# Kernel tuning notes

Hardware: AMD Instinct MI355X
Metric: run time of the kernel (lower is better)

The kernel has to match this reference:

```python
import jax, jax.numpy as jnp
import numpy as np

N = 100000    # nodes
E = 1600000   # edges (avg degree 16)
IN = 128      # input feature dim
D = 32        # per-head hidden dim
H = 4         # heads for hidden layers
C = 16        # num_classes (final per-head dim)
NEG = 0.2     # leaky_relu negative slope


def setup_inputs() -> dict:
    key = jax.random.key(0)
    ks = jax.random.split(key, 14)
    s = jnp.float32(0.05)
    f32 = jnp.float32
    inp = {
        "inputs": jax.random.normal(ks[0], (N, IN), f32),
        "src": jax.random.randint(ks[1], (E,), 0, N),
        "dst": jax.random.randint(ks[2], (E,), 0, N),
        # layer 0: IN -> (H, D), no residual
        "W0": jax.random.normal(ks[3], (IN, H * D), f32) * s,
        "al0": jax.random.normal(ks[4], (H, D), f32) * s,
        "ar0": jax.random.normal(ks[5], (H, D), f32) * s,
        # layer 1: H*D -> (H, D), identity residual (dims match)
        "W1": jax.random.normal(ks[6], (H * D, H * D), f32) * s,
        "al1": jax.random.normal(ks[7], (H, D), f32) * s,
        "ar1": jax.random.normal(ks[8], (H, D), f32) * s,
        # final layer: H*D -> (1, C), linear residual projection
        "W2": jax.random.normal(ks[9], (H * D, 1 * C), f32) * s,
        "al2": jax.random.normal(ks[10], (1, C), f32) * s,
        "ar2": jax.random.normal(ks[11], (1, C), f32) * s,
        "resW2": jax.random.normal(ks[12], (H * D, 1 * C), f32) * s,
    }
    return inp


def gat_conv(h, W, al, ar, src, dst, n_heads, out_dim, res=None, act=None):
    # h: (N, F_in) -> out: (N, n_heads, out_dim)
    feat = (h @ W).reshape(N, n_heads, out_dim)            # (N,H,D)
    el = jnp.sum(feat * al, axis=-1)                       # (N,H)
    er = jnp.sum(feat * ar, axis=-1)                       # (N,H)
    e = jax.nn.leaky_relu(el[src] + er[dst], NEG)          # (E,H)
    # softmax over incoming edges per destination node
    emax = jax.ops.segment_max(e, dst, num_segments=N)     # (N,H)
    ex = jnp.exp(e - emax[dst])                            # (E,H)
    den = jax.ops.segment_sum(ex, dst, num_segments=N)     # (N,H)
    alpha = ex / den[dst]                                  # (E,H)
    msg = feat[src] * alpha[:, :, None]                    # (E,H,D) -- dominant traffic
    out = jax.ops.segment_sum(msg, dst, num_segments=N)    # (N,H,D)
    if res is not None:
        out = out + res
    if act is not None:
        out = act(out)
    return out


def reference(inputs, src, dst, W0, al0, ar0, W1, al1, ar1, W2, al2, ar2, resW2):
    # hidden layer 0 (no residual), GATConv activation = elu, then flatten + relu
    h = gat_conv(inputs, W0, al0, ar0, src, dst, H, D, res=None, act=jax.nn.elu)
    h = jax.nn.relu(h.reshape(N, H * D))
    # hidden layer 1, identity residual (in == H*D)
    res1 = h.reshape(N, H, D)
    h = gat_conv(h, W1, al1, ar1, src, dst, H, D, res=res1, act=jax.nn.elu)
    h = jax.nn.relu(h.reshape(N, H * D))
    # output layer: 1 head, linear residual projection, no activation, mean over heads
    res2 = (h @ resW2).reshape(N, 1, C)
    out = gat_conv(h, W2, al2, ar2, src, dst, 1, C, res=res2, act=None)
    return out.mean(axis=1)                                # (N, C)
```

## Files before the change

### kernel.cpp

```cpp
#include <hip/hip_runtime.h>

#define N_NODES 100000
#define N_EDGES 1600000
#define IN_F    128
#define NEG_SLOPE 0.2f
#define NBUCK   512
#define BCAP    5120
#define PCHUNK  4096
#define PGRID   391
#define GEMMGRID 1563

typedef __attribute__((ext_vector_type(8))) short bf16x8;
typedef __attribute__((ext_vector_type(4))) float f32x4;

__device__ __forceinline__ float bf2f(unsigned short u) {
    return __uint_as_float(((unsigned int)u) << 16);
}

__device__ __forceinline__ unsigned short f2bf(float f) {
    unsigned int u = __float_as_uint(f);
    u += 0x7FFFu + ((u >> 16) & 1u);
    return (unsigned short)(u >> 16);
}

__global__ __launch_bounds__(256) void init_pack(int* __restrict__ bcursor,
                                                 const float* __restrict__ W0,
                                                 const float* __restrict__ W1,
                                                 const float* __restrict__ W2,
                                                 const float* __restrict__ rW2,
                                                 unsigned short* __restrict__ W0p,
                                                 unsigned short* __restrict__ W1p,
                                                 unsigned short* __restrict__ W2p) {
    const int t = threadIdx.x;
    if (blockIdx.x < 2) {
        int i = blockIdx.x * 256 + t;
        if (i < NBUCK) bcursor[i] = i * BCAP;
        return;
    }
    int gid = (blockIdx.x - 2) * 256 + t;
    const float* W;
    unsigned short* Wp;
    int idx, ncols;
    if (gid < 16384)      { W = W0; Wp = W0p; idx = gid;          ncols = 128; }
    else if (gid < 32768) { W = W1; Wp = W1p; idx = gid - 16384;  ncols = 128; }
    else                  { W = W2; Wp = W2p; idx = gid - 32768;  ncols = 32;  }
    int j  = idx & 7;
    int l  = (idx >> 3) & 63;
    int kt = (idx >> 9) & 3;
    int nt = idx >> 11;
    int k  = kt * 32 + (l >> 4) * 8 + j;
    int n  = nt * 16 + (l & 15);
    float v;
    if (ncols == 128) v = W[k * 128 + n];
    else              v = (n < 16) ? W[k * 16 + n] : rW2[k * 16 + (n - 16)];
    Wp[idx] = f2bf(v);
}

__global__ __launch_bounds__(256) void part_gemm0(const int* __restrict__ src,
                                                  const int* __restrict__ dst,
                                                  int* __restrict__ bcursor,
                                                  unsigned int* __restrict__ pe, int nE,
                                                  const float* __restrict__ A,
                                                  const unsigned short* __restrict__ Wp,
                                                  const float* __restrict__ al,
                                                  const float* __restrict__ ar,
                                                  unsigned short* __restrict__ featb,
                                                  float* __restrict__ el,
                                                  float* __restrict__ er,
                                                  int nrows) {
    __shared__ int hist[NBUCK];
    __shared__ int lstart[NBUCK];
    __shared__ int gbase[NBUCK];
    __shared__ int curB[NBUCK];
    __shared__ int s[NBUCK];
    __shared__ unsigned int reorder[PCHUNK];

    const int t = threadIdx.x;

    if (blockIdx.x < PGRID) {
        const int start = blockIdx.x * PCHUNK;

        hist[t] = 0; hist[t + 256] = 0;
        __syncthreads();
#pragma unroll
        for (int j = 0; j < PCHUNK / 256; ++j) {
            int e = start + j * 256 + t;
            if (e < nE) atomicAdd(&hist[dst[e] >> 8], 1);
        }
        __syncthreads();
        const int c0 = hist[t];
        const int c1 = hist[t + 256];
        s[t] = c0; s[t + 256] = c1;
        __syncthreads();
#pragma unroll
        for (int off = 1; off <= 256; off <<= 1) {
            int x0 = (t >= off) ? s[t - off] : 0;
            int x1 = s[t + 256 - off];
            __syncthreads();
            s[t] += x0; s[t + 256] += x1;
            __syncthreads();
        }
        lstart[t]       = s[t] - c0;
        lstart[t + 256] = s[t + 256] - c1;
        curB[t]         = s[t] - c0;
        curB[t + 256]   = s[t + 256] - c1;
        gbase[t]        = c0 ? atomicAdd(&bcursor[t],       c0) : 0;
        gbase[t + 256]  = c1 ? atomicAdd(&bcursor[t + 256], c1) : 0;
        __syncthreads();

#pragma unroll
        for (int j = 0; j < PCHUNK / 256; ++j) {
            int e = start + j * 256 + t;
            if (e < nE) {
                int d  = dst[e];
                int sv = src[e];
                int b  = d >> 8;
                int pos = atomicAdd(&curB[b], 1);
                reorder[pos] = ((unsigned)sv << 8) | ((unsigned)d & 255u);
            }
        }
        __syncthreads();

        for (int b = t; b < NBUCK; b += 256) {
            int st = lstart[b];
            int en = curB[b];
            int gb = gbase[b];
            for (int k = st; k < en; ++k)
                pe[gb + (k - st)] = reorder[k];
        }
    } else {
        const int bid  = blockIdx.x - PGRID;
        const int wv   = t >> 6;
        const int lane = t & 63;
        const int q    = lane >> 4;
        const int m    = lane & 15;
        const int rb   = bid * 64 + wv * 16;
        const int arow = rb + m;
        const bool rok = arow < nrows;
        const float* Ar = A + (size_t)arow * IN_F;

        f32x4 acc[8];
#pragma unroll
        for (int nt = 0; nt < 8; ++nt) acc[nt] = (f32x4){0.f, 0.f, 0.f, 0.f};

#pragma unroll
        for (int kt = 0; kt < 4; ++kt) {
            bf16x8 afr = (bf16x8){0, 0, 0, 0, 0, 0, 0, 0};
            if (rok) {
                float4 v0 = *(const float4*)(Ar + kt * 32 + q * 8);
                float4 v1 = *(const float4*)(Ar + kt * 32 + q * 8 + 4);
                afr[0] = (short)f2bf(v0.x); afr[1] = (short)f2bf(v0.y);
                afr[2] = (short)f2bf(v0.z); afr[3] = (short)f2bf(v0.w);
                afr[4] = (short)f2bf(v1.x); afr[5] = (short)f2bf(v1.y);
                afr[6] = (short)f2bf(v1.z); afr[7] = (short)f2bf(v1.w);
            }
#pragma unroll
            for (int nt = 0; nt < 8; ++nt) {
                bf16x8 bfr = *(const bf16x8*)(Wp + ((size_t)(nt * 4 + kt) * 64 + lane) * 8);
                acc[nt] = __builtin_amdgcn_mfma_f32_16x16x32_bf16(afr, bfr, acc[nt], 0, 0, 0);
            }
        }

        float pel[16], per[16];
#pragma unroll
        for (int i = 0; i < 16; ++i) { pel[i] = 0.f; per[i] = 0.f; }

#pragma unroll
        for (int nt = 0; nt < 8; ++nt) {
            const int col = nt * 16 + m;
            const float alv = al[col];
            const float arv = ar[col];
            const int h = nt >> 1;
#pragma unroll
            for (int reg = 0; reg < 4; ++reg) {
                int row = rb + q * 4 + reg;
                float a = acc[nt][reg];
                if (row < nrows) featb[(size_t)row * 128 + col] = f2bf(a);
                pel[reg * 4 + h] += a * alv;
                per[reg * 4 + h] += a * arv;
            }
        }
#pragma unroll
        for (int sh = 8; sh > 0; sh >>= 1) {
#pragma unroll
            for (int i = 0; i < 16; ++i) {
                pel[i] += __shfl_down(pel[i], sh);
                per[i] += __shfl_down(per[i], sh);
            }
        }
        if (m == 0) {
#pragma unroll
            for (int reg = 0; reg < 4; ++reg) {
                int row = rb + q * 4 + reg;
                if (row < nrows) {
#pragma unroll
                    for (int h = 0; h < 4; ++h) {
                        el[row * 4 + h] = pel[reg * 4 + h];
                        er[row * 4 + h] = per[reg * 4 + h];
                    }
                }
            }
        }
    }
}

__global__ __launch_bounds__(256) void bucket_finalize(const unsigned int* __restrict__ pe,
                                                       const int* __restrict__ bcursor,
                                                       int* __restrict__ rowptr,
                                                       int* __restrict__ deg,
                                                       int* __restrict__ sorted_src) {
    __shared__ int deg_l[256];
    __shared__ int s[256];
    __shared__ int cur[256];

    const int b  = blockIdx.x;
    const int t  = threadIdx.x;
    const int base = b * BCAP;
    const int cnt  = bcursor[b] - base;
    const int n    = b * 256 + t;

    deg_l[t] = 0;
    __syncthreads();
    for (int i = t; i < cnt; i += 256)
        atomicAdd(&deg_l[pe[base + i] & 255u], 1);
    __syncthreads();

    const int dv = deg_l[t];
    s[t] = dv;
    __syncthreads();
#pragma unroll
    for (int off = 1; off < 256; off <<= 1) {
        int x = (t >= off) ? s[t - off] : 0;
        __syncthreads();
        s[t] += x;
        __syncthreads();
    }
    const int off_l = s[t] - dv;
    if (n < N_NODES) {
        rowptr[n] = base + off_l;
        deg[n]    = dv;
    }
    cur[t] = off_l;
    __syncthreads();

    for (int i = t; i < cnt; i += 256) {
        unsigned int ed = pe[base + i];
        int pos = atomicAdd(&cur[ed & 255u], 1);
        sorted_src[base + pos] = (int)(ed >> 8);
    }
}

__global__ __launch_bounds__(256) void gemm128_mfma_bf16(const unsigned short* __restrict__ Ab,
                                                         const unsigned short* __restrict__ Wp,
                                                         const float* __restrict__ al,
                                                         const float* __restrict__ ar,
                                                         unsigned short* __restrict__ featb,
                                                         float* __restrict__ el,
                                                         float* __restrict__ er,
                                                         int nrows) {
    const int t    = threadIdx.x;
    const int wv   = t >> 6;
    const int lane = t & 63;
    const int q    = lane >> 4;
    const int m    = lane & 15;
    const int rb   = blockIdx.x * 64 + wv * 16;
    const int arow = rb + m;
    const bool rok = arow < nrows;
    const unsigned short* Ar = Ab + (size_t)arow * IN_F;

    f32x4 acc[8];
#pragma unroll
    for (int nt = 0; nt < 8; ++nt) acc[nt] = (f32x4){0.f, 0.f, 0.f, 0.f};

#pragma unroll
    for (int kt = 0; kt < 4; ++kt) {
        bf16x8 afr = (bf16x8){0, 0, 0, 0, 0, 0, 0, 0};
        if (rok) afr = *(const bf16x8*)(Ar + kt * 32 + q * 8);
#pragma unroll
        for (int nt = 0; nt < 8; ++nt) {
            bf16x8 bfr = *(const bf16x8*)(Wp + ((size_t)(nt * 4 + kt) * 64 + lane) * 8);
            acc[nt] = __builtin_amdgcn_mfma_f32_16x16x32_bf16(afr, bfr, acc[nt], 0, 0, 0);
        }
    }

    float pel[16], per[16];
#pragma unroll
    for (int i = 0; i < 16; ++i) { pel[i] = 0.f; per[i] = 0.f; }

#pragma unroll
    for (int nt = 0; nt < 8; ++nt) {
        const int col = nt * 16 + m;
        const float alv = al[col];
        const float arv = ar[col];
        const int h = nt >> 1;
#pragma unroll
        for (int reg = 0; reg < 4; ++reg) {
            int row = rb + q * 4 + reg;
            float a = acc[nt][reg];
            if (row < nrows) featb[(size_t)row * 128 + col] = f2bf(a);
            pel[reg * 4 + h] += a * alv;
            per[reg * 4 + h] += a * arv;
        }
    }
#pragma unroll
    for (int sh = 8; sh > 0; sh >>= 1) {
#pragma unroll
        for (int i = 0; i < 16; ++i) {
            pel[i] += __shfl_down(pel[i], sh);
            per[i] += __shfl_down(per[i], sh);
        }
    }
    if (m == 0) {
#pragma unroll
        for (int reg = 0; reg < 4; ++reg) {
            int row = rb + q * 4 + reg;
            if (row < nrows) {
#pragma unroll
                for (int h = 0; h < 4; ++h) {
                    el[row * 4 + h] = pel[reg * 4 + h];
                    er[row * 4 + h] = per[reg * 4 + h];
                }
            }
        }
    }
}

__global__ __launch_bounds__(256) void gemm16_mfma(const unsigned short* __restrict__ Ab,
                                                   const unsigned short* __restrict__ Wp,
                                                   const float* __restrict__ al,
                                                   const float* __restrict__ ar,
                                                   unsigned short* __restrict__ feat2b,
                                                   float* __restrict__ res2,
                                                   float* __restrict__ el,
                                                   float* __restrict__ er,
                                                   int nrows) {
    const int t    = threadIdx.x;
    const int wv   = t >> 6;
    const int lane = t & 63;
    const int q    = lane >> 4;
    const int m    = lane & 15;
    const int rb   = blockIdx.x * 64 + wv * 16;
    const int arow = rb + m;
    const bool rok = arow < nrows;
    const unsigned short* Ar = Ab + (size_t)arow * IN_F;

    f32x4 acc0 = (f32x4){0.f, 0.f, 0.f, 0.f};
    f32x4 acc1 = (f32x4){0.f, 0.f, 0.f, 0.f};

#pragma unroll
    for (int kt = 0; kt < 4; ++kt) {
        bf16x8 afr = (bf16x8){0, 0, 0, 0, 0, 0, 0, 0};
        if (rok) afr = *(const bf16x8*)(Ar + kt * 32 + q * 8);
        bf16x8 b0 = *(const bf16x8*)(Wp + ((size_t)(0 * 4 + kt) * 64 + lane) * 8);
        bf16x8 b1 = *(const bf16x8*)(Wp + ((size_t)(1 * 4 + kt) * 64 + lane) * 8);
        acc0 = __builtin_amdgcn_mfma_f32_16x16x32_bf16(afr, b0, acc0, 0, 0, 0);
        acc1 = __builtin_amdgcn_mfma_f32_16x16x32_bf16(afr, b1, acc1, 0, 0, 0);
    }

    float pel[4], per[4];
    const float alv = al[m];
    const float arv = ar[m];
#pragma unroll
    for (int reg = 0; reg < 4; ++reg) {
        int row = rb + q * 4 + reg;
        float a = acc0[reg];
        if (row < nrows) {
            feat2b[(size_t)row * 16 + m] = f2bf(a);
            res2[(size_t)row * 16 + m]   = acc1[reg];
        }
        pel[reg] = a * alv;
        per[reg] = a * arv;
    }
#pragma unroll
    for (int sh = 8; sh > 0; sh >>= 1) {
#pragma unroll
        for (int reg = 0; reg < 4; ++reg) {
            pel[reg] += __shfl_down(pel[reg], sh);
            per[reg] += __shfl_down(per[reg], sh);
        }
    }
    if (m == 0) {
#pragma unroll
        for (int reg = 0; reg < 4; ++reg) {
            int row = rb + q * 4 + reg;
            if (row < nrows) { el[row] = pel[reg]; er[row] = per[reg]; }
        }
    }
}

__global__ __launch_bounds__(256) void gat_agg128(const int* __restrict__ rowptr,
                                                  const int* __restrict__ deg,
                                                  const int* __restrict__ sorted_src,
                                                  const float* __restrict__ el,
                                                  const float* __restrict__ er,
                                                  const unsigned short* __restrict__ featb,
                                                  const unsigned short* __restrict__ resb,
                                                  unsigned short* __restrict__ outb) {
    __shared__ int   sS[4][64];
    __shared__ float sW[4][64][4];

    const int wv   = threadIdx.x >> 6;
    const int lane = threadIdx.x & 63;
    const int nd   = blockIdx.x * 4 + wv;

    const int dg = deg[nd];
    const int r0 = rowptr[nd];
    const int h  = lane >> 4;
    const float4 er4 = *(const float4*)(er + nd * 4);

    float den = 0.f;
    float ax = 0.f, ay = 0.f;

    for (int base = 0; base < dg; base += 64) {
        int m = dg - base; if (m > 64) m = 64;
        if (lane < m) {
            int s = sorted_src[r0 + base + lane];
            sS[wv][lane] = s;
            float4 e4 = *(const float4*)(el + s * 4);
            float4 w;
            float v;
            v = e4.x + er4.x; v = v > 0.f ? v : NEG_SLOPE * v; w.x = __expf(v);
            v = e4.y + er4.y; v = v > 0.f ? v : NEG_SLOPE * v; w.y = __expf(v);
            v = e4.z + er4.z; v = v > 0.f ? v : NEG_SLOPE * v; w.z = __expf(v);
            v = e4.w + er4.w; v = v > 0.f ? v : NEG_SLOPE * v; w.w = __expf(v);
            *(float4*)(&sW[wv][lane][0]) = w;
        }
        int i = 0;
        for (; i + 3 < m; i += 4) {
            int s0 = sS[wv][i];
            int s1 = sS[wv][i + 1];
            int s2 = sS[wv][i + 2];
            int s3 = sS[wv][i + 3];
            float w0 = sW[wv][i][h];
            float w1 = sW[wv][i + 1][h];
            float w2 = sW[wv][i + 2][h];
            float w3 = sW[wv][i + 3][h];
            ushort2 u0 = *((const ushort2*)(featb + (size_t)s0 * 128) + lane);
            ushort2 u1 = *((const ushort2*)(featb + (size_t)s1 * 128) + lane);
            ushort2 u2 = *((const ushort2*)(featb + (size_t)s2 * 128) + lane);
            ushort2 u3 = *((const ushort2*)(featb + (size_t)s3 * 128) + lane);
            den += w0 + w1 + w2 + w3;
            ax += w0 * bf2f(u0.x);
            ay += w0 * bf2f(u0.y);
            ax += w1 * bf2f(u1.x);
            ay += w1 * bf2f(u1.y);
            ax += w2 * bf2f(u2.x);
            ay += w2 * bf2f(u2.y);
            ax += w3 * bf2f(u3.x);
            ay += w3 * bf2f(u3.y);
        }
        for (; i < m; ++i) {
            int s   = sS[wv][i];
            float w = sW[wv][i][h];
            den += w;
            ushort2 u = *((const ushort2*)(featb + (size_t)s * 128) + lane);
            ax += w * bf2f(u.x);
            ay += w * bf2f(u.y);
        }
    }

    float scale = den > 0.f ? 1.f / den : 0.f;
    float ox = ax * scale, oy = ay * scale;
    size_t o0 = (size_t)nd * 128 + lane * 2;
    if (resb) {
        ushort2 rv = *(const ushort2*)(resb + o0);
        ox += bf2f(rv.x);
        oy += bf2f(rv.y);
    }
    ox = fmaxf(ox, 0.f);
    oy = fmaxf(oy, 0.f);
    ushort2 ou;
    ou.x = f2bf(ox);
    ou.y = f2bf(oy);
    *(ushort2*)(outb + o0) = ou;
}

__global__ __launch_bounds__(256) void gat_agg16(const int* __restrict__ rowptr,
                                                 const int* __restrict__ deg,
                                                 const int* __restrict__ sorted_src,
                                                 const float* __restrict__ el,
                                                 const float* __restrict__ er,
                                                 const unsigned short* __restrict__ feat2b,
                                                 const float* __restrict__ res,
                                                 float* __restrict__ out) {
    __shared__ int   sS[4][64];
    __shared__ float sW[4][64];

    const int wv   = threadIdx.x >> 6;
    const int lane = threadIdx.x & 63;
    const int nd   = blockIdx.x * 4 + (threadIdx.x >> 6);
    const int g    = lane >> 3;
    const int f2   = (lane & 7) * 2;

    const int dg = deg[nd];
    const int r0 = rowptr[nd];
    const float erd = er[nd];

    float ax = 0.f, ay = 0.f, den = 0.f;

    for (int base = 0; base < dg; base += 64) {
        int m = dg - base; if (m > 64) m = 64;
        if (lane < m) {
            int s = sorted_src[r0 + base + lane];
            sS[wv][lane] = s;
            float v = el[s] + erd;
            v = v > 0.f ? v : NEG_SLOPE * v;
            sW[wv][lane] = __expf(v);
        }
        for (int i = g; i < m; i += 8) {
            int s   = sS[wv][i];
            float w = sW[wv][i];
            den += w;
            ushort2 u = *(const ushort2*)(feat2b + (size_t)s * 16 + f2);
            ax += w * bf2f(u.x);
            ay += w * bf2f(u.y);
        }
    }

    ax += __shfl_down(ax, 32); ay += __shfl_down(ay, 32); den += __shfl_down(den, 32);
    ax += __shfl_down(ax, 16); ay += __shfl_down(ay, 16); den += __shfl_down(den, 16);
    ax += __shfl_down(ax, 8);  ay += __shfl_down(ay, 8);  den += __shfl_down(den, 8);

    if (lane < 8) {
        float scale = den > 0.f ? 1.f / den : 0.f;
        size_t o0 = (size_t)nd * 16 + f2;
        float2 o;
        o.x = ax * scale + res[o0];
        o.y = ay * scale + res[o0 + 1];
        *(float2*)(out + o0) = o;
    }
}

extern "C" void kernel_launch(void* const* d_in, const int* in_sizes, int n_in,
                              void* d_out, int out_size, void* d_ws, size_t ws_size,
                              hipStream_t stream) {
    const float* inputs = (const float*)d_in[0];
    const int*   src    = (const int*)d_in[1];
    const int*   dst    = (const int*)d_in[2];
    const float* W0     = (const float*)d_in[3];
    const float* al0    = (const float*)d_in[4];
    const float* ar0    = (const float*)d_in[5];
    const float* W1     = (const float*)d_in[6];
    const float* al1    = (const float*)d_in[7];
    const float* ar1    = (const float*)d_in[8];
    const float* W2     = (const float*)d_in[9];
    const float* al2    = (const float*)d_in[10];
    const float* ar2    = (const float*)d_in[11];
    const float* resW2  = (const float*)d_in[12];
    float* out = (float*)d_out;

    const size_t NF = (size_t)N_NODES * 128;
    float* ws   = (float*)d_ws;
    float* el   = ws;
    float* er   = el + (size_t)N_NODES * 4;
    float* res2 = er + (size_t)N_NODES * 4;
    unsigned short* hbufb  = (unsigned short*)(res2 + (size_t)N_NODES * 16);
    unsigned short* featb  = hbufb + NF;
    unsigned short* feat2b = featb + NF;
    unsigned short* W0p    = feat2b + (size_t)N_NODES * 16;
    unsigned short* W1p    = W0p + 16384;
    unsigned short* W2p    = W1p + 16384;
    int* iws = (int*)(W2p + 8192);
    unsigned int* pe = (unsigned int*)iws;
    int* sorted_src  = iws + NBUCK * BCAP;
    int* deg         = sorted_src + NBUCK * BCAP;
    int* rowptr      = deg + N_NODES;
    int* bcursor     = rowptr + N_NODES;

    dim3 blk(256);
    int aggGrid = N_NODES / 4;

    init_pack<<<162, blk, 0, stream>>>(bcursor, W0, W1, W2, resW2, W0p, W1p, W2p);
    part_gemm0<<<PGRID + GEMMGRID, blk, 0, stream>>>(src, dst, bcursor, pe, N_EDGES,
                                                     inputs, W0p, al0, ar0, featb,
                                                     el, er, N_NODES);
    bucket_finalize<<<PGRID, blk, 0, stream>>>(pe, bcursor, rowptr, deg, sorted_src);

    gat_agg128<<<aggGrid, blk, 0, stream>>>(rowptr, deg, sorted_src, el, er, featb,
                                            nullptr, hbufb);

    gemm128_mfma_bf16<<<GEMMGRID, blk, 0, stream>>>(hbufb, W1p, al1, ar1, featb,
                                                    el, er, N_NODES);
    gat_agg128<<<aggGrid, blk, 0, stream>>>(rowptr, deg, sorted_src, el, er, featb,
                                            hbufb, hbufb);

    gemm16_mfma<<<GEMMGRID, blk, 0, stream>>>(hbufb, W2p, al2, ar2, feat2b, res2,
                                              el, er, N_NODES);
    gat_agg16<<<aggGrid, blk, 0, stream>>>(rowptr, deg, sorted_src, el, er, feat2b,
                                           res2, out);
}
```

Before: 385.3 us.

## Software-pipeline neighbor feature gathers in 16-edge batches using readlane indices

```diff
diff --git a/kernel.cpp b/kernel.cpp
--- a/kernel.cpp
+++ b/kernel.cpp
@@ -388,6 +388,21 @@
     }
 }
 
+#define LOAD16(B, START, CNT)                                                  \
+    {                                                                          \
+        _Pragma("unroll")                                                      \
+        for (int jg_ = 0; jg_ < 16; jg_ += 4) {                                \
+            if (jg_ < (CNT)) {                                                 \
+                _Pragma("unroll")                                              \
+                for (int k_ = 0; k_ < 4; ++k_) {                               \
+                    int sj_ = __builtin_amdgcn_readlane(s_own, (START) + jg_ + k_); \
+                    const unsigned short* rp_ = featb + (size_t)sj_ * 128;     \
+                    (B)[jg_ + k_] = *((const ushort2*)rp_ + lane);             \
+                }                                                              \
+            }                                                                  \
+        }                                                                      \
+    }
+
 __global__ __launch_bounds__(256) void gat_agg128(const int* __restrict__ rowptr,
                                                   const int* __restrict__ deg,
                                                   const int* __restrict__ sorted_src,
@@ -396,7 +411,6 @@
                                                   const unsigned short* __restrict__ featb,
                                                   const unsigned short* __restrict__ resb,
                                                   unsigned short* __restrict__ outb) {
-    __shared__ int   sS[4][64];
     __shared__ float sW[4][64][4];
 
     const int wv   = threadIdx.x >> 6;
@@ -413,49 +427,51 @@
 
     for (int base = 0; base < dg; base += 64) {
         int m = dg - base; if (m > 64) m = 64;
+
+        int s_own = 0;
+        if (lane < m) s_own = sorted_src[r0 + base + lane];
+
+        ushort2 u[16], v[16];
+        int c = m < 16 ? m : 16;
+        LOAD16(u, 0, c)
+
+        float4 w4;
         if (lane < m) {
-            int s = sorted_src[r0 + base + lane];
-            sS[wv][lane] = s;
-            float4 e4 = *(const float4*)(el + s * 4);
-            float4 w;
-            float v;
-            v = e4.x + er4.x; v = v > 0.f ? v : NEG_SLOPE * v; w.x = __expf(v);
-            v = e4.y + er4.y; v = v > 0.f ? v : NEG_SLOPE * v; w.y = __expf(v);
-            v = e4.z + er4.z; v = v > 0.f ? v : NEG_SLOPE * v; w.z = __expf(v);
-            v = e4.w + er4.w; v = v > 0.f ? v : NEG_SLOPE * v; w.w = __expf(v);
-            *(float4*)(&sW[wv][lane][0]) = w;
-        }
+            float4 e4 = *(const float4*)(el + s_own * 4);
+            float t_;
+            t_ = e4.x + er4.x; t_ = t_ > 0.f ? t_ : NEG_SLOPE * t_; w4.x = __expf(t_);
+            t_ = e4.y + er4.y; t_ = t_ > 0.f ? t_ : NEG_SLOPE * t_; w4.y = __expf(t_);
+            t_ = e4.z + er4.z; t_ = t_ > 0.f ? t_ : NEG_SLOPE * t_; w4.z = __expf(t_);
+            t_ = e4.w + er4.w; t_ = t_ > 0.f ? t_ : NEG_SLOPE * t_; w4.w = __expf(t_);
+        } else {
+            w4.x = 0.f; w4.y = 0.f; w4.z = 0.f; w4.w = 0.f;
+        }
+        *(float4*)(&sW[wv][lane][0]) = w4;
+
         int i = 0;
-        for (; i + 3 < m; i += 4) {
-            int s0 = sS[wv][i];
-            int s1 = sS[wv][i + 1];
-            int s2 = sS[wv][i + 2];
-            int s3 = sS[wv][i + 3];
-            float w0 = sW[wv][i][h];
-            float w1 = sW[wv][i + 1][h];
-            float w2 = sW[wv][i + 2][h];
-            float w3 = sW[wv][i + 3][h];
-            ushort2 u0 = *((const ushort2*)(featb + (size_t)s0 * 128) + lane);
-            ushort2 u1 = *((const ushort2*)(featb + (size_t)s1 * 128) + lane);
-            ushort2 u2 = *((const ushort2*)(featb + (size_t)s2 * 128) + lane);
-            ushort2 u3 = *((const ushort2*)(featb + (size_t)s3 * 128) + lane);
-            den += w0 + w1 + w2 + w3;
-            ax += w0 * bf2f(u0.x);
-            ay += w0 * bf2f(u0.y);
-            ax += w1 * bf2f(u1.x);
-            ay += w1 * bf2f(u1.y);
-            ax += w2 * bf2f(u2.x);
-            ay += w2 * bf2f(u2.y);
-            ax += w3 * bf2f(u3.x);
-            ay += w3 * bf2f(u3.y);
-        }
-        for (; i < m; ++i) {
-            int s   = sS[wv][i];
-            float w = sW[wv][i][h];
-            den += w;
-            ushort2 u = *((const ushort2*)(featb + (size_t)s * 128) + lane);
-            ax += w * bf2f(u.x);
-            ay += w * bf2f(u.y);
+        while (true) {
+            int in_ = i + c;
+            int cn = m - in_; if (cn > 16) cn = 16;
+            if (cn > 0) LOAD16(v, in_, cn)
+
+            const float* wb = &sW[wv][i][h];
+#pragma unroll
+            for (int jg = 0; jg < 16; jg += 4) {
+                if (jg < c) {
+#pragma unroll
+                    for (int k = 0; k < 4; ++k) {
+                        float w = wb[(jg + k) * 4];
+                        ushort2 uu = u[jg + k];
+                        den += w;
+                        ax += w * bf2f(uu.x);
+                        ay += w * bf2f(uu.y);
+                    }
+                }
+            }
+            if (cn <= 0) break;
+#pragma unroll
+            for (int k = 0; k < 16; ++k) u[k] = v[k];
+            i = in_; c = cn;
         }
     }
 
```

New measurement: 392.1 us. No clear change (+1.7%).
